# Performance work log

Hardware: AMD Instinct MI355X
Metric: run time of the kernel (lower is better)

## Reference

```python
import jax, jax.numpy as jnp
import numpy as np

B, S, N = 1, 256, 384
MSA_S, Z_D = 64, 128
H, C_H = 8, 32
C_OPM = 32
INF = 1e9

def ln(x, w, b):
    mu = jnp.mean(x, -1, keepdims=True)
    var = jnp.mean(jnp.square(x - mu), -1, keepdims=True)
    return (x - mu) * jax.lax.rsqrt(var + 1e-5) * w + b

def setup_inputs() -> dict:
    key = jax.random.key(0)
    ks = jax.random.split(key, 16)
    def lin(k, out_d, in_d):
        return jax.random.normal(k, (out_d, in_d), jnp.float32) / np.sqrt(in_d)
    return {
        "z": jax.random.normal(ks[0], (B, N, N, Z_D), jnp.float32),
        "m": jax.random.normal(ks[1], (B, S, N, MSA_S), jnp.float32),
        "token_mask": jnp.ones((B, N, N), jnp.float32),
        "msa_mask": jnp.ones((B, S, N), jnp.float32),
        "norm_z_w": jnp.ones((Z_D,), jnp.float32), "norm_z_b": jnp.zeros((Z_D,), jnp.float32),
        "proj_z_w": lin(ks[2], H, Z_D),
        "norm_m_w": jnp.ones((MSA_S,), jnp.float32), "norm_m_b": jnp.zeros((MSA_S,), jnp.float32),
        "proj_m_w": lin(ks[3], H * C_H, MSA_S),
        "proj_g_w": lin(ks[4], H * C_H, MSA_S),
        "pwa_proj_o_w": lin(ks[5], MSA_S, H * C_H),
        "trans_norm_w": jnp.ones((MSA_S,), jnp.float32), "trans_norm_b": jnp.zeros((MSA_S,), jnp.float32),
        "fc1_w": lin(ks[6], 4 * MSA_S, MSA_S),
        "fc2_w": lin(ks[7], 4 * MSA_S, MSA_S),
        "fc3_w": lin(ks[8], MSA_S, 4 * MSA_S),
        "opm_norm_w": jnp.ones((MSA_S,), jnp.float32), "opm_norm_b": jnp.zeros((MSA_S,), jnp.float32),
        "proj_a_w": lin(ks[9], C_OPM, MSA_S),
        "proj_b_w": lin(ks[10], C_OPM, MSA_S),
        "opm_proj_o_w": lin(ks[11], Z_D, C_OPM * C_OPM),
        "opm_proj_o_b": jnp.zeros((Z_D,), jnp.float32),
    }

def reference(z, m, token_mask, msa_mask,
              norm_z_w, norm_z_b, proj_z_w,
              norm_m_w, norm_m_b, proj_m_w, proj_g_w, pwa_proj_o_w,
              trans_norm_w, trans_norm_b, fc1_w, fc2_w, fc3_w,
              opm_norm_w, opm_norm_b, proj_a_w, proj_b_w, opm_proj_o_w, opm_proj_o_b):
    # --- PairWeightedAveraging: pair-biased, gated MSA row attention ---
    b_full = ln(z, norm_z_w, norm_z_b) @ proj_z_w.T                     # [B,N,N,H]
    bias = jnp.transpose(b_full, (0, 3, 1, 2)) + (1.0 - token_mask[:, None]) * (-INF)
    w = jax.nn.softmax(bias, axis=-1)                                   # [B,H,N,N]
    mn = ln(m, norm_m_w, norm_m_b)
    v = (mn @ proj_m_w.T).reshape(B, S, N, H, C_H)                      # [B,S,N,H,c]
    g = jax.nn.sigmoid(mn @ proj_g_w.T)                                 # [B,S,N,H*c]
    o = jnp.einsum('bhij,bsjhd->bsihd', w, v).reshape(B, S, N, H * C_H)
    m = m + (g * o) @ pwa_proj_o_w.T
    # --- MSA transition (SwiGLU) ---
    tn = ln(m, trans_norm_w, trans_norm_b)
    m = m + (jax.nn.silu(tn @ fc1_w.T) * (tn @ fc2_w.T)) @ fc3_w.T
    # --- OuterProductMean -> pair update ---
    mk = msa_mask[..., None]                                            # [B,S,N,1]
    on = ln(m, opm_norm_w, opm_norm_b)
    a = (on @ proj_a_w.T) * mk                                          # [B,S,N,c]
    bb = (on @ proj_b_w.T) * mk                                         # [B,S,N,c]
    num_mask = jnp.clip(jnp.einsum('bsi,bsj->bij', msa_mask, msa_mask), 1.0, None)[..., None]
    opm = jnp.einsum('bsic,bsjd->bijcd', a, bb).reshape(B, N, N, C_OPM * C_OPM) / num_mask
    z = z + opm @ opm_proj_o_w.T + opm_proj_o_b
    return (z, m)
```

## Files before the change

kernel.cpp:

```cpp
#include <hip/hip_runtime.h>
#include <math.h>

constexpr int NRES = 384;
constexpr int NSEQ = 256;
constexpr int DM   = 64;
constexpr int DZ   = 128;
constexpr int NH   = 8;
constexpr int DH   = 32;
constexpr int HC   = NH * DH;
constexpr int DOP  = 32;
constexpr int FF   = 4 * DM;

constexpr int NPAIR = NRES * NRES;
constexpr int NROWS = NSEQ * NRES;
constexpr int ZTOT  = NPAIR * DZ;
constexpr int SD    = NSEQ * DH;
constexpr int ICHUNK = 96;

typedef unsigned short ushort_t;
typedef __attribute__((ext_vector_type(8))) short short8;
typedef __attribute__((ext_vector_type(4))) float f32x4;

__device__ __forceinline__ float wred_sum(float v) {
    #pragma unroll
    for (int off = 32; off; off >>= 1) v += __shfl_xor(v, off, 64);
    return v;
}
__device__ __forceinline__ float sigm(float x) { return 1.0f / (1.0f + expf(-x)); }
__device__ __forceinline__ ushort_t cvt_bf(float f) {
    unsigned u = __float_as_uint(f);
    unsigned r = (u + 0x7FFFu + ((u >> 16) & 1u)) >> 16;
    return (ushort_t)r;
}
__device__ __forceinline__ float cvt_f(ushort_t h) {
    return __uint_as_float(((unsigned)h) << 16);
}
__device__ __forceinline__ f32x4 mfma16(short8 a, short8 b, f32x4 c) {
    return __builtin_amdgcn_mfma_f32_16x16x32_bf16(a, b, c, 0, 0, 0);
}
__device__ __forceinline__ void gld16(const ushort_t* g, ushort_t* l) {
    __builtin_amdgcn_global_load_lds(
        (const __attribute__((address_space(1))) unsigned int*)g,
        (__attribute__((address_space(3))) unsigned int*)l, 16, 0, 0);
}

__global__ __launch_bounds__(256) void k_prep(const float* __restrict__ f1,
                                              const float* __restrict__ f2,
                                              const float* __restrict__ f3,
                                              const float* __restrict__ opW,
                                              const float* __restrict__ pmw,
                                              const float* __restrict__ pgw,
                                              const float* __restrict__ pow_,
                                              const float* __restrict__ paw,
                                              const float* __restrict__ pbw,
                                              const float* __restrict__ pzw,
                                              ushort_t* __restrict__ f1b,
                                              ushort_t* __restrict__ f2b,
                                              ushort_t* __restrict__ f3b,
                                              ushort_t* __restrict__ opWb,
                                              ushort_t* __restrict__ pmwb,
                                              ushort_t* __restrict__ pgwb,
                                              ushort_t* __restrict__ powb,
                                              ushort_t* __restrict__ abwb,
                                              ushort_t* __restrict__ pzwb) {
    int i = blockIdx.x * 256 + threadIdx.x;
    opWb[i] = cvt_bf(opW[i]);
    if (i < FF * DM) {
        f1b[i] = cvt_bf(f1[i]);
        f2b[i] = cvt_bf(f2[i]);
        f3b[i] = cvt_bf(f3[i]);
    }
    if (i < HC * DM) {
        pmwb[i] = cvt_bf(pmw[i]);
        pgwb[i] = cvt_bf(pgw[i]);
        powb[i] = cvt_bf(pow_[i]);
    }
    if (i < 2 * DOP * DM) {
        abwb[i] = cvt_bf(i < DOP * DM ? paw[i] : pbw[i - DOP * DM]);
    }
    if (i < 16 * DZ) {
        pzwb[i] = (i < NH * DZ) ? cvt_bf(pzw[i]) : (ushort_t)0;
    }
}

__global__ __launch_bounds__(256) void k_biassm(const float* __restrict__ z,
                                                const float* __restrict__ nzw,
                                                const float* __restrict__ nzb,
                                                const ushort_t* __restrict__ pzwb,
                                                const float* __restrict__ tmask,
                                                ushort_t* __restrict__ wsb) {
    int i = blockIdx.x;
    __shared__ ushort_t Azl[128][136];
    __shared__ ushort_t Bl[16][136];
    __shared__ float ob[8][388];
    __shared__ float wln[128], bln[128];
    int t = threadIdx.x;
    if (t < 128) { wln[t] = nzw[t]; bln[t] = nzb[t]; }
    int wave = t >> 6, lane = t & 63;
    int lk = (lane >> 4) * 8, lr = lane & 15;
    int wr = wave * 32;
    for (int idx = t * 8; idx < 16 * DZ; idx += 256 * 8) {
        int row = idx >> 7, col = idx & 127;
        *(short8*)&Bl[row][col] = *(const short8*)&pzwb[idx];
    }
    __syncthreads();
    for (int c = 0; c < 3; c++) {
        {
            int jl = t >> 1, cb = (t & 1) * 64;
            const float* src = &z[((size_t)i * NRES + c * 128 + jl) * DZ + cb];
            float4 v[16];
            float s1 = 0.0f, s2 = 0.0f;
            #pragma unroll
            for (int q = 0; q < 16; q++) {
                v[q] = *(const float4*)&src[q * 4];
                s1 += v[q].x + v[q].y + v[q].z + v[q].w;
                s2 += v[q].x * v[q].x + v[q].y * v[q].y + v[q].z * v[q].z + v[q].w * v[q].w;
            }
            s1 += __shfl_xor(s1, 1, 64);
            s2 += __shfl_xor(s2, 1, 64);
            float mu = s1 * (1.0f / 128.0f);
            float var = s2 * (1.0f / 128.0f) - mu * mu;
            float rs = rsqrtf(var + 1e-5f);
            #pragma unroll
            for (int q = 0; q < 8; q++) {
                float4 xa = v[2 * q], xb = v[2 * q + 1];
                int base = cb + q * 8;
                short8 o;
                o[0] = (short)cvt_bf((xa.x - mu) * rs * wln[base + 0] + bln[base + 0]);
                o[1] = (short)cvt_bf((xa.y - mu) * rs * wln[base + 1] + bln[base + 1]);
                o[2] = (short)cvt_bf((xa.z - mu) * rs * wln[base + 2] + bln[base + 2]);
                o[3] = (short)cvt_bf((xa.w - mu) * rs * wln[base + 3] + bln[base + 3]);
                o[4] = (short)cvt_bf((xb.x - mu) * rs * wln[base + 4] + bln[base + 4]);
                o[5] = (short)cvt_bf((xb.y - mu) * rs * wln[base + 5] + bln[base + 5]);
                o[6] = (short)cvt_bf((xb.z - mu) * rs * wln[base + 6] + bln[base + 6]);
                o[7] = (short)cvt_bf((xb.w - mu) * rs * wln[base + 7] + bln[base + 7]);
                *(short8*)&Azl[jl][base] = o;
            }
        }
        __syncthreads();
        f32x4 acc[2] = {};
        #pragma unroll
        for (int ks = 0; ks < 4; ks++) {
            short8 b = *(const short8*)&Bl[lr][ks * 32 + lk];
            short8 a0 = *(const short8*)&Azl[wr + lr][ks * 32 + lk];
            short8 a1 = *(const short8*)&Azl[wr + 16 + lr][ks * 32 + lk];
            acc[0] = mfma16(a0, b, acc[0]);
            acc[1] = mfma16(a1, b, acc[1]);
        }
        if (lr < NH) {
            #pragma unroll
            for (int ri = 0; ri < 2; ri++) {
                int jb = c * 128 + wr + 16 * ri + (lane >> 4) * 4;
                #pragma unroll
                for (int r = 0; r < 4; r++)
                    ob[lr][jb + r] = acc[ri][r];
            }
        }
        __syncthreads();
    }
    int h = wave * 2 + (lane >> 5);
    int l32 = lane & 31;
    int jb = l32 * 12;
    const float* tm = &tmask[(size_t)i * NRES];
    float vals[12];
    float mx = -1e30f;
    #pragma unroll
    for (int q = 0; q < 12; q++) {
        float v = ob[h][jb + q] + (1.0f - tm[jb + q]) * (-1e9f);
        vals[q] = v;
        mx = fmaxf(mx, v);
    }
    #pragma unroll
    for (int off = 16; off; off >>= 1) mx = fmaxf(mx, __shfl_xor(mx, off, 64));
    float sum = 0.0f;
    #pragma unroll
    for (int q = 0; q < 12; q++) { vals[q] = expf(vals[q] - mx); sum += vals[q]; }
    #pragma unroll
    for (int off = 16; off; off >>= 1) sum += __shfl_xor(sum, off, 64);
    float inv = 1.0f / sum;
    ushort_t* o = &wsb[(size_t)h * NPAIR + (size_t)i * NRES + jb];
    #pragma unroll
    for (int q = 0; q < 12; q++) o[q] = cvt_bf(vals[q] * inv);
}

__global__ __launch_bounds__(256) void k_ln64(const float* __restrict__ src,
                                              const float* __restrict__ lw,
                                              const float* __restrict__ lb,
                                              ushort_t* __restrict__ dst) {
    int wave = threadIdx.x >> 6, lane = threadIdx.x & 63;
    int r = blockIdx.x * 4 + wave;
    float x = src[(size_t)r * DM + lane];
    float mu = wred_sum(x) * (1.0f / 64.0f);
    float d = x - mu;
    float var = wred_sum(d * d) * (1.0f / 64.0f);
    dst[(size_t)r * DM + lane] = cvt_bf(d * rsqrtf(var + 1e-5f) * lw[lane] + lb[lane]);
}

__global__ __launch_bounds__(256) void k_vproj_mfma(const ushort_t* __restrict__ A,
                                                    const ushort_t* __restrict__ Bt,
                                                    ushort_t* __restrict__ vtt) {
    int m0 = blockIdx.y * 64, n0c = blockIdx.x * 64;
    __shared__ ushort_t Al[64][40];
    __shared__ ushort_t Bl[64][40];
    __shared__ ushort_t ot[64][72];
    int t = threadIdx.x;
    int srow = t >> 2, sko = (t & 3) * 8;
    int wave = t >> 6, lane = t & 63;
    int wr = (wave >> 1) * 32, wc = (wave & 1) * 32;
    int lk = (lane >> 4) * 8, lr = lane & 15;
    f32x4 acc[2][2] = {};
    for (int k0 = 0; k0 < DM; k0 += 32) {
        *(short8*)&Al[srow][sko] = *(const short8*)&A[(size_t)(m0 + srow) * DM + k0 + sko];
        *(short8*)&Bl[srow][sko] = *(const short8*)&Bt[(size_t)(n0c + srow) * DM + k0 + sko];
        __syncthreads();
        short8 a0 = *(const short8*)&Al[wr + lr][lk];
        short8 a1 = *(const short8*)&Al[wr + 16 + lr][lk];
        short8 b0 = *(const short8*)&Bl[wc + lr][lk];
        short8 b1 = *(const short8*)&Bl[wc + 16 + lr][lk];
        acc[0][0] = mfma16(a0, b0, acc[0][0]);
        acc[0][1] = mfma16(a0, b1, acc[0][1]);
        acc[1][0] = mfma16(a1, b0, acc[1][0]);
        acc[1][1] = mfma16(a1, b1, acc[1][1]);
        __syncthreads();
    }
    #pragma unroll
    for (int ri = 0; ri < 2; ri++)
        #pragma unroll
        for (int ci = 0; ci < 2; ci++) {
            int rowb = wr + 16 * ri + (lane >> 4) * 4;
            int colb = wc + 16 * ci + lr;
            #pragma unroll
            for (int r = 0; r < 4; r++)
                ot[colb][rowb + r] = cvt_bf(acc[ri][ci][r]);
        }
    __syncthreads();
    int s = m0 / NRES, n0 = m0 % NRES;
    int h0 = n0c >> 5;
    int orow = t >> 2, seg = (t & 3) * 16;
    short8 v0 = *(const short8*)&ot[orow][seg];
    short8 v1 = *(const short8*)&ot[orow][seg + 8];
    int hh = orow >> 5, dd = orow & 31;
    ushort_t* dst = &vtt[(((size_t)(h0 + hh) * SD) + s * DH + dd) * NRES + n0 + seg];
    *(short8*)&dst[0] = v0;
    *(short8*)&dst[8] = v1;
}

__global__ __launch_bounds__(256) void k_tr(const ushort_t* __restrict__ src,
                                            ushort_t* __restrict__ dst,
                                            int R, int C) {
    size_t bs = (size_t)R * C;
    const ushort_t* s = src + blockIdx.z * bs;
    ushort_t* d = dst + blockIdx.z * bs;
    int r0 = blockIdx.y * 64, c0 = blockIdx.x * 64;
    __shared__ ushort_t tile[64][72];
    int t = threadIdx.x;
    int tr = t >> 2, tc = (t & 3) * 16;
    *(short8*)&tile[tr][tc]     = *(const short8*)&s[(size_t)(r0 + tr) * C + c0 + tc];
    *(short8*)&tile[tr][tc + 8] = *(const short8*)&s[(size_t)(r0 + tr) * C + c0 + tc + 8];
    __syncthreads();
    short8 o0, o1;
    #pragma unroll
    for (int i = 0; i < 8; i++) {
        o0[i] = (short)tile[tc + i][tr];
        o1[i] = (short)tile[tc + 8 + i][tr];
    }
    *(short8*)&d[(size_t)(c0 + tr) * R + r0 + tc]     = o0;
    *(short8*)&d[(size_t)(c0 + tr) * R + r0 + tc + 8] = o1;
}

__global__ __launch_bounds__(256) void k_attn_mfma(const ushort_t* __restrict__ wsb,
                                                   const ushort_t* __restrict__ vtt,
                                                   ushort_t* __restrict__ otb2) {
    int h = blockIdx.z;
    const ushort_t* A  = wsb + (size_t)h * NPAIR;
    const ushort_t* Bt = vtt + (size_t)h * SD * NRES;
    int m0 = blockIdx.y * 128, n0 = blockIdx.x * 128;
    __shared__ ushort_t Al[128 * 32];
    __shared__ ushort_t Bl[128 * 32];
    int t = threadIdx.x;
    int w = t >> 6, lane = t & 63;
    int wr = (w >> 1) * 64, wc = (w & 1) * 64;
    int lq = lane >> 4, lr = lane & 15;
    int rS = w * 16 + (lane >> 2);
    int cqs = (((lane & 3) ^ ((rS >> 1) & 3)) << 3);
    f32x4 acc[4][4] = {};
    for (int k0 = 0; k0 < NRES; k0 += 32) {
        gld16(&A [(size_t)(m0 + rS)      * NRES + k0 + cqs], &Al[(w * 16) * 32]);
        gld16(&A [(size_t)(m0 + 64 + rS) * NRES + k0 + cqs], &Al[(64 + w * 16) * 32]);
        gld16(&Bt[(size_t)(n0 + rS)      * NRES + k0 + cqs], &Bl[(w * 16) * 32]);
        gld16(&Bt[(size_t)(n0 + 64 + rS) * NRES + k0 + cqs], &Bl[(64 + w * 16) * 32]);
        __syncthreads();
        short8 af[4], bf2[4];
        #pragma unroll
        for (int i = 0; i < 4; i++) {
            int ra = wr + 16 * i + lr;
            int rb = wc + 16 * i + lr;
            af[i]  = *(const short8*)&Al[ra * 32 + ((lq ^ ((ra >> 1) & 3)) << 3)];
            bf2[i] = *(const short8*)&Bl[rb * 32 + ((lq ^ ((rb >> 1) & 3)) << 3)];
        }
        #pragma unroll
        for (int ri = 0; ri < 4; ri++)
            #pragma unroll
            for (int ci = 0; ci < 4; ci++)
                acc[ri][ci] = mfma16(af[ri], bf2[ci], acc[ri][ci]);
        __syncthreads();
    }
    #pragma unroll
    for (int ri = 0; ri < 4; ri++)
        #pragma unroll
        for (int ci = 0; ci < 4; ci++) {
            int row0 = m0 + wr + 16 * ri + (lane >> 4) * 4;
            int col  = n0 + wc + 16 * ci + lr;
            int s = col >> 5, dd = col & 31;
            #pragma unroll
            for (int r = 0; r < 4; r++)
                otb2[((size_t)s * NRES + row0 + r) * HC + h * DH + dd] = cvt_bf(acc[ri][ci][r]);
        }
}

__global__ __launch_bounds__(256) void k_gateout(const ushort_t* __restrict__ A,
                                                 const ushort_t* __restrict__ Bg,
                                                 const ushort_t* __restrict__ otb2,
                                                 const ushort_t* __restrict__ Bo,
                                                 const float* __restrict__ m,
                                                 float* __restrict__ mout) {
    int m0 = blockIdx.x * 64;
    __shared__ ushort_t Al[64][72];
    __shared__ ushort_t Bl[64][72];
    __shared__ ushort_t go[64][264];
    int t = threadIdx.x;
    int srow = t >> 2, sko = (t & 3) * 16;
    int wave = t >> 6, lane = t & 63;
    int wr = (wave >> 1) * 32, wc = (wave & 1) * 32;
    int lk = (lane >> 4) * 8, lr = lane & 15;
    {
        const ushort_t* arow = &A[(size_t)(m0 + srow) * DM + sko];
        *(short8*)&Al[srow][sko]     = *(const short8*)&arow[0];
        *(short8*)&Al[srow][sko + 8] = *(const short8*)&arow[8];
    }
    __syncthreads();
    short8 a[2][2];
    a[0][0] = *(const short8*)&Al[wr + lr][lk];
    a[0][1] = *(const short8*)&Al[wr + lr][32 + lk];
    a[1][0] = *(const short8*)&Al[wr + 16 + lr][lk];
    a[1][1] = *(const short8*)&Al[wr + 16 + lr][32 + lk];
    for (int nq = 0; nq < 4; nq++) {
        __syncthreads();
        {
            const ushort_t* brow = &Bg[(size_t)(nq * 64 + srow) * DM + sko];
            *(short8*)&Bl[srow][sko]     = *(const short8*)&brow[0];
            *(short8*)&Bl[srow][sko + 8] = *(const short8*)&brow[8];
        }
        __syncthreads();
        f32x4 acc[2][2] = {};
        #pragma unroll
        for (int ks = 0; ks < 2; ks++) {
            short8 b0 = *(const short8*)&Bl[wc + lr][ks * 32 + lk];
            short8 b1 = *(const short8*)&Bl[wc + 16 + lr][ks * 32 + lk];
            acc[0][0] = mfma16(a[0][ks], b0, acc[0][0]);
            acc[0][1] = mfma16(a[0][ks], b1, acc[0][1]);
            acc[1][0] = mfma16(a[1][ks], b0, acc[1][0]);
            acc[1][1] = mfma16(a[1][ks], b1, acc[1][1]);
        }
        #pragma unroll
        for (int ri = 0; ri < 2; ri++)
            #pragma unroll
            for (int ci = 0; ci < 2; ci++) {
                int lrow = wr + 16 * ri + (lane >> 4) * 4;
                int col  = nq * 64 + wc + 16 * ci + lr;
                #pragma unroll
                for (int r = 0; r < 4; r++) {
                    float ov = cvt_f(otb2[(size_t)(m0 + lrow + r) * HC + col]);
                    go[lrow + r][col] = cvt_bf(sigm(acc[ri][ci][r]) * ov);
                }
            }
    }
    f32x4 acc[2][2] = {};
    for (int k0 = 0; k0 < HC; k0 += 32) {
        __syncthreads();
        *(short8*)&Bl[t >> 2][(t & 3) * 8] = *(const short8*)&Bo[(size_t)(t >> 2) * HC + k0 + (t & 3) * 8];
        __syncthreads();
        short8 a0 = *(const short8*)&go[wr + lr][k0 + lk];
        short8 a1 = *(const short8*)&go[wr + 16 + lr][k0 + lk];
        short8 b0 = *(const short8*)&Bl[wc + lr][lk];
        short8 b1 = *(const short8*)&Bl[wc + 16 + lr][lk];
        acc[0][0] = mfma16(a0, b0, acc[0][0]);
        acc[0][1] = mfma16(a0, b1, acc[0][1]);
        acc[1][0] = mfma16(a1, b0, acc[1][0]);
        acc[1][1] = mfma16(a1, b1, acc[1][1]);
    }
    #pragma unroll
    for (int ri = 0; ri < 2; ri++)
        #pragma unroll
        for (int ci = 0; ci < 2; ci++) {
            int row0 = m0 + wr + 16 * ri + (lane >> 4) * 4;
            int col  = wc + 16 * ci + lr;
            #pragma unroll
            for (int r = 0; r < 4; r++) {
                size_t idx = (size_t)(row0 + r) * DM + col;
                mout[idx] = m[idx] + acc[ri][ci][r];
            }
        }
}

__global__ __launch_bounds__(256) void k_fctrans(const ushort_t* __restrict__ A,
                                                 const ushort_t* __restrict__ B1,
                                                 const ushort_t* __restrict__ B2,
                                                 const ushort_t* __restrict__ B3,
                                                 float* __restrict__ mio) {
    int m0 = blockIdx.x * 64;
    __shared__ ushort_t Al[64][72];
    __shared__ ushort_t B1l[64][72];
    __shared__ ushort_t B2l[64][72];
    __shared__ ushort_t hhl[64][264];
    int t = threadIdx.x;
    int srow = t >> 2, sko = (t & 3) * 16;
    int wave = t >> 6, lane = t & 63;
    int wr = (wave >> 1) * 32, wc = (wave & 1) * 32;
    int lk = (lane >> 4) * 8, lr = lane & 15;
    {
        const ushort_t* arow = &A[(size_t)(m0 + srow) * DM + sko];
        *(short8*)&Al[srow][sko]     = *(const short8*)&arow[0];
        *(short8*)&Al[srow][sko + 8] = *(const short8*)&arow[8];
    }
    __syncthreads();
    short8 a[2][2];
    a[0][0] = *(const short8*)&Al[wr + lr][lk];
    a[0][1] = *(const short8*)&Al[wr + lr][32 + lk];
    a[1][0] = *(const short8*)&Al[wr + 16 + lr][lk];
    a[1][1] = *(const short8*)&Al[wr + 16 + lr][32 + lk];
    for (int nq = 0; nq < 4; nq++) {
        __syncthreads();
        {
            const ushort_t* b1r = &B1[(size_t)(nq * 64 + srow) * DM + sko];
            const ushort_t* b2r = &B2[(size_t)(nq * 64 + srow) * DM + sko];
            *(short8*)&B1l[srow][sko]     = *(const short8*)&b1r[0];
            *(short8*)&B1l[srow][sko + 8] = *(const short8*)&b1r[8];
            *(short8*)&B2l[srow][sko]     = *(const short8*)&b2r[0];
            *(short8*)&B2l[srow][sko + 8] = *(const short8*)&b2r[8];
        }
        __syncthreads();
        f32x4 acc1[2][2] = {}, acc2[2][2] = {};
        #pragma unroll
        for (int ks = 0; ks < 2; ks++) {
            short8 p0 = *(const short8*)&B1l[wc + lr][ks * 32 + lk];
            short8 p1 = *(const short8*)&B1l[wc + 16 + lr][ks * 32 + lk];
            short8 q0 = *(const short8*)&B2l[wc + lr][ks * 32 + lk];
            short8 q1 = *(const short8*)&B2l[wc + 16 + lr][ks * 32 + lk];
            acc1[0][0] = mfma16(a[0][ks], p0, acc1[0][0]);
            acc1[0][1] = mfma16(a[0][ks], p1, acc1[0][1]);
            acc1[1][0] = mfma16(a[1][ks], p0, acc1[1][0]);
            acc1[1][1] = mfma16(a[1][ks], p1, acc1[1][1]);
            acc2[0][0] = mfma16(a[0][ks], q0, acc2[0][0]);
            acc2[0][1] = mfma16(a[0][ks], q1, acc2[0][1]);
            acc2[1][0] = mfma16(a[1][ks], q0, acc2[1][0]);
            acc2[1][1] = mfma16(a[1][ks], q1, acc2[1][1]);
        }
        #pragma unroll
        for (int ri = 0; ri < 2; ri++)
            #pragma unroll
            for (int ci = 0; ci < 2; ci++) {
                int lrow = wr + 16 * ri + (lane >> 4) * 4;
                int col  = nq * 64 + wc + 16 * ci + lr;
                #pragma unroll
                for (int r = 0; r < 4; r++) {
                    float a1v = acc1[ri][ci][r], a2v = acc2[ri][ci][r];
                    hhl[lrow + r][col] = cvt_bf(a1v * sigm(a1v) * a2v);
                }
            }
    }
    f32x4 acc[2][2] = {};
    for (int k0 = 0; k0 < FF; k0 += 32) {
        __syncthreads();
        *(short8*)&B1l[t >> 2][(t & 3) * 8] = *(const short8*)&B3[(size_t)(t >> 2) * FF + k0 + (t & 3) * 8];
        __syncthreads();
        short8 a0 = *(const short8*)&hhl[wr + lr][k0 + lk];
        short8 a1 = *(const short8*)&hhl[wr + 16 + lr][k0 + lk];
        short8 b0 = *(const short8*)&B1l[wc + lr][lk];
        short8 b1 = *(const short8*)&B1l[wc + 16 + lr][lk];
        acc[0][0] = mfma16(a0, b0, acc[0][0]);
        acc[0][1] = mfma16(a0, b1, acc[0][1]);
        acc[1][0] = mfma16(a1, b0, acc[1][0]);
        acc[1][1] = mfma16(a1, b1, acc[1][1]);
    }
    #pragma unroll
    for (int ri = 0; ri < 2; ri++)
        #pragma unroll
        for (int ci = 0; ci < 2; ci++) {
            int row0 = m0 + wr + 16 * ri + (lane >> 4) * 4;
            int col  = wc + 16 * ci + lr;
            #pragma unroll
            for (int r = 0; r < 4; r++)
                mio[(size_t)(row0 + r) * DM + col] += acc[ri][ci][r];
        }
}

__global__ __launch_bounds__(256) void k_ab_mfma(const ushort_t* __restrict__ A,
                                                 const ushort_t* __restrict__ Bt,
                                                 const float* __restrict__ smask,
                                                 ushort_t* __restrict__ abuf,
                                                 ushort_t* __restrict__ bbuf) {
    int m0 = blockIdx.x * 64;
    __shared__ ushort_t Al[64][40];
    __shared__ ushort_t Bl[64][40];
    int t = threadIdx.x;
    int srow = t >> 2, sko = (t & 3) * 8;
    int wave = t >> 6, lane = t & 63;
    int wr = (wave >> 1) * 32, wc = (wave & 1) * 32;
    int lk = (lane >> 4) * 8, lr = lane & 15;
    f32x4 acc[2][2] = {};
    for (int k0 = 0; k0 < DM; k0 += 32) {
        *(short8*)&Al[srow][sko] = *(const short8*)&A[(size_t)(m0 + srow) * DM + k0 + sko];
        *(short8*)&Bl[srow][sko] = *(const short8*)&Bt[(size_t)srow * DM + k0 + sko];
        __syncthreads();
        short8 a0 = *(const short8*)&Al[wr + lr][lk];
        short8 a1 = *(const short8*)&Al[wr + 16 + lr][lk];
        short8 b0 = *(const short8*)&Bl[wc + lr][lk];
        short8 b1 = *(const short8*)&Bl[wc + 16 + lr][lk];
        acc[0][0] = mfma16(a0, b0, acc[0][0]);
        acc[0][1] = mfma16(a0, b1, acc[0][1]);
        acc[1][0] = mfma16(a1, b0, acc[1][0]);
        acc[1][1] = mfma16(a1, b1, acc[1][1]);
        __syncthreads();
    }
    #pragma unroll
    for (int ri = 0; ri < 2; ri++)
        #pragma unroll
        for (int ci = 0; ci < 2; ci++) {
            int row0 = m0 + wr + 16 * ri + (lane >> 4) * 4;
            int col  = wc + 16 * ci + lr;
            #pragma unroll
            for (int r = 0; r < 4; r++) {
                int rr = row0 + r;
                int s = rr / NRES, n = rr % NRES;
                float v = acc[ri][ci][r] * smask[rr];
                if (col < DOP)
                    abuf[(size_t)s * (NRES * DOP) + n * DOP + col] = cvt_bf(v);
                else
                    bbuf[(size_t)s * (NRES * DOP) + n * DOP + (col - DOP)] = cvt_bf(v);
            }
        }
}

__global__ __launch_bounds__(256) void k_msum(const float* __restrict__ smask,
                                              float* __restrict__ msum) {
    int i0 = blockIdx.y * 64, j0 = blockIdx.x * 64;
    __shared__ float As[16][64];
    __shared__ float Bs[16][64];
    int t = threadIdx.x;
    int ty = t >> 4, tx = t & 15;
    float acc[4][4] = {};
    for (int k0 = 0; k0 < NSEQ; k0 += 16) {
        int kk = t >> 4, x4 = (t & 15) * 4;
        *(float4*)&As[kk][x4] = *(const float4*)&smask[(size_t)(k0 + kk) * NRES + i0 + x4];
        *(float4*)&Bs[kk][x4] = *(const float4*)&smask[(size_t)(k0 + kk) * NRES + j0 + x4];
        __syncthreads();
        #pragma unroll
        for (int k = 0; k < 16; k++) {
            float4 a4 = *(const float4*)&As[k][ty * 4];
            float4 b4 = *(const float4*)&Bs[k][tx * 4];
            float ar[4] = {a4.x, a4.y, a4.z, a4.w};
            float br[4] = {b4.x, b4.y, b4.z, b4.w};
            #pragma unroll
            for (int i2 = 0; i2 < 4; i2++)
                #pragma unroll
                for (int j2 = 0; j2 < 4; j2++)
                    acc[i2][j2] += ar[i2] * br[j2];
        }
        __syncthreads();
    }
    #pragma unroll
    for (int r = 0; r < 4; r++) {
        float4 o4 = make_float4(fmaxf(acc[r][0], 1.0f), fmaxf(acc[r][1], 1.0f),
                                fmaxf(acc[r][2], 1.0f), fmaxf(acc[r][3], 1.0f));
        *(float4*)&msum[(size_t)(i0 + ty * 4 + r) * NRES + j0 + tx * 4] = o4;
    }
}

__global__ __launch_bounds__(256) void k_opm_mfma(const ushort_t* __restrict__ At,
                                                  const ushort_t* __restrict__ Bt,
                                                  ushort_t* __restrict__ opmc) {
    int m0 = blockIdx.y * 128;
    int n0 = blockIdx.x * 128;
    __shared__ ushort_t Al[128 * 32];
    __shared__ ushort_t Bl[128 * 32];
    int t = threadIdx.x;
    int w = t >> 6, lane = t & 63;
    int wr = (w >> 1) * 64, wc = (w & 1) * 64;
    int lq = lane >> 4, lr = lane & 15;
    int rS = w * 16 + (lane >> 2);
    int cqs = (((lane & 3) ^ ((rS >> 1) & 3)) << 3);
    f32x4 acc[4][4] = {};
    for (int k0 = 0; k0 < NSEQ; k0 += 32) {
        gld16(&At[(size_t)(m0 + rS)      * NSEQ + k0 + cqs], &Al[(w * 16) * 32]);
        gld16(&At[(size_t)(m0 + 64 + rS) * NSEQ + k0 + cqs], &Al[(64 + w * 16) * 32]);
        gld16(&Bt[(size_t)(n0 + rS)      * NSEQ + k0 + cqs], &Bl[(w * 16) * 32]);
        gld16(&Bt[(size_t)(n0 + 64 + rS) * NSEQ + k0 + cqs], &Bl[(64 + w * 16) * 32]);
        __syncthreads();
        short8 af[4], bf2[4];
        #pragma unroll
        for (int i = 0; i < 4; i++) {
            int ra = wr + 16 * i + lr;
            int rb = wc + 16 * i + lr;
            af[i]  = *(const short8*)&Al[ra * 32 + ((lq ^ ((ra >> 1) & 3)) << 3)];
            bf2[i] = *(const short8*)&Bl[rb * 32 + ((lq ^ ((rb >> 1) & 3)) << 3)];
        }
        #pragma unroll
        for (int ri = 0; ri < 4; ri++)
            #pragma unroll
            for (int ci = 0; ci < 4; ci++)
                acc[ri][ci] = mfma16(af[ri], bf2[ci], acc[ri][ci]);
        __syncthreads();
    }
    #pragma unroll
    for (int ri = 0; ri < 4; ri++)
        #pragma unroll
        for (int ci = 0; ci < 4; ci++) {
            int mb = m0 + wr + 16 * ri + (lane >> 4) * 4;
            int n  = n0 + wc + 16 * ci + lr;
            int j = n >> 5, dd = n & 31;
            #pragma unroll
            for (int r = 0; r < 4; r++) {
                int mm = mb + r;
                int il = mm >> 5, c = mm & 31;
                opmc[((size_t)(il * NRES + j) << 10) + (c << 5) + dd] = cvt_bf(acc[ri][ci][r]);
            }
        }
}

__global__ __launch_bounds__(256) void k_proj_mfma(const ushort_t* __restrict__ A,
                                                   const ushort_t* __restrict__ Bt,
                                                   const float* __restrict__ opB,
                                                   const float* __restrict__ msum,
                                                   const float* __restrict__ zin,
                                                   float* __restrict__ zout,
                                                   int ib) {
    int m0 = blockIdx.x * 128;
    __shared__ ushort_t Al[128 * 32];
    __shared__ ushort_t Bl[128 * 32];
    int t = threadIdx.x;
    int w = t >> 6, lane = t & 63;
    int wr = (w >> 1) * 64, wc = (w & 1) * 64;
    int lq = lane >> 4, lr = lane & 15;
    int rS = w * 16 + (lane >> 2);
    int cqs = (((lane & 3) ^ ((rS >> 1) & 3)) << 3);
    f32x4 acc[4][4] = {};
    for (int k0 = 0; k0 < 1024; k0 += 32) {
        gld16(&A [(size_t)(m0 + rS)      * 1024 + k0 + cqs], &Al[(w * 16) * 32]);
        gld16(&A [(size_t)(m0 + 64 + rS) * 1024 + k0 + cqs], &Al[(64 + w * 16) * 32]);
        gld16(&Bt[(size_t)(rS)           * 1024 + k0 + cqs], &Bl[(w * 16) * 32]);
        gld16(&Bt[(size_t)(64 + rS)      * 1024 + k0 + cqs], &Bl[(64 + w * 16) * 32]);
        __syncthreads();
        short8 af[4], bf2[4];
        #pragma unroll
        for (int i = 0; i < 4; i++) {
            int ra = wr + 16 * i + lr;
            int rb = wc + 16 * i + lr;
            af[i]  = *(const short8*)&Al[ra * 32 + ((lq ^ ((ra >> 1) & 3)) << 3)];
            bf2[i] = *(const short8*)&Bl[rb * 32 + ((lq ^ ((rb >> 1) & 3)) << 3)];
        }
        #pragma unroll
        for (int ri = 0; ri < 4; ri++)
            #pragma unroll
            for (int ci = 0; ci < 4; ci++)
                acc[ri][ci] = mfma16(af[ri], bf2[ci], acc[ri][ci]);
        __syncthreads();
    }
    #pragma unroll
    for (int ri = 0; ri < 4; ri++)
        #pragma unroll
        for (int ci = 0; ci < 4; ci++) {
            int row0 = m0 + wr + 16 * ri + (lane >> 4) * 4;
            int col  = wc + 16 * ci + lr;
            #pragma unroll
            for (int r = 0; r < 4; r++) {
                size_t G = (size_t)ib * NRES + row0 + r;
                float inv = 1.0f / msum[G];
                zout[G * DZ + col] = zin[G * DZ + col] + acc[ri][ci][r] * inv + opB[col];
            }
        }
}

extern "C" void kernel_launch(void* const* d_in, const int* in_sizes, int n_in,
                              void* d_out, int out_size, void* d_ws, size_t ws_size,
                              hipStream_t stream) {
    const float* z     = (const float*)d_in[0];
    const float* m     = (const float*)d_in[1];
    const float* tmask = (const float*)d_in[2];
    const float* smask = (const float*)d_in[3];
    const float* nzw   = (const float*)d_in[4];
    const float* nzb   = (const float*)d_in[5];
    const float* pzw   = (const float*)d_in[6];
    const float* nmw   = (const float*)d_in[7];
    const float* nmb   = (const float*)d_in[8];
    const float* pmw   = (const float*)d_in[9];
    const float* pgw   = (const float*)d_in[10];
    const float* pow_  = (const float*)d_in[11];
    const float* tnw   = (const float*)d_in[12];
    const float* tnb_  = (const float*)d_in[13];
    const float* f1    = (const float*)d_in[14];
    const float* f2    = (const float*)d_in[15];
    const float* f3    = (const float*)d_in[16];
    const float* onw   = (const float*)d_in[17];
    const float* onb   = (const float*)d_in[18];
    const float* paw   = (const float*)d_in[19];
    const float* pbw   = (const float*)d_in[20];
    const float* opW   = (const float*)d_in[21];
    const float* opB   = (const float*)d_in[22];

    float* zout = (float*)d_out;
    float* mout = zout + ZTOT;

    char* W = (char*)d_ws;
    ushort_t* wsb  = (ushort_t*)(W + 4718592);
    ushort_t* mnb  = (ushort_t*)(W + 7077888);
    ushort_t* vtR  = (ushort_t*)(W + 19660800);
    ushort_t* vtt  = (ushort_t*)(W + 69992448);
    ushort_t* otb2 = (ushort_t*)(W + 120324096);
    float*    msum = (float*)(W + 170655744);
    ushort_t* f1b  = (ushort_t*)(W + 171245568);
    ushort_t* f2b  = (ushort_t*)(W + 171278336);
    ushort_t* f3b  = (ushort_t*)(W + 171311104);
    ushort_t* opWb = (ushort_t*)(W + 171343872);
    ushort_t* pmwb = (ushort_t*)(W + 171606016);
    ushort_t* pgwb = (ushort_t*)(W + 171638784);
    ushort_t* powb = (ushort_t*)(W + 171671552);
    ushort_t* abwb = (ushort_t*)(W + 171704320);
    ushort_t* pzwb = (ushort_t*)(W + 171712512);
    ushort_t* tn_bf = vtt;
    ushort_t* onb_bf = mnb;
    ushort_t* abuf = (ushort_t*)(W + 69992448 + 12582912);
    ushort_t* bbuf = (ushort_t*)(W + 69992448 + 18874368);
    ushort_t* abt  = otb2;
    ushort_t* bbt  = (ushort_t*)(W + 120324096 + 6291456);
    ushort_t* opmc = vtR;

    k_prep<<<512, 256, 0, stream>>>(f1, f2, f3, opW, pmw, pgw, pow_, paw, pbw, pzw,
                                    f1b, f2b, f3b, opWb, pmwb, pgwb, powb, abwb, pzwb);

    k_biassm<<<NRES, 256, 0, stream>>>(z, nzw, nzb, pzwb, tmask, wsb);
    k_ln64<<<NROWS / 4, 256, 0, stream>>>(m, nmw, nmb, mnb);
    k_vproj_mfma<<<dim3(HC / 64, NROWS / 64), 256, 0, stream>>>(mnb, pmwb, vtt);
    k_attn_mfma<<<dim3(SD / 128, NRES / 128, NH), 256, 0, stream>>>(wsb, vtt, otb2);
    k_gateout<<<NROWS / 64, 256, 0, stream>>>(mnb, pgwb, otb2, powb, m, mout);

    k_ln64<<<NROWS / 4, 256, 0, stream>>>(mout, tnw, tnb_, tn_bf);
    k_fctrans<<<NROWS / 64, 256, 0, stream>>>(tn_bf, f1b, f2b, f3b, mout);

    k_ln64<<<NROWS / 4, 256, 0, stream>>>(mout, onw, onb, onb_bf);
    k_ab_mfma<<<NROWS / 64, 256, 0, stream>>>(onb_bf, abwb, smask, abuf, bbuf);
    k_tr<<<dim3((NRES * DOP) / 64, NSEQ / 64, 2), 256, 0, stream>>>(abuf, abt, NSEQ, NRES * DOP);
    k_msum<<<dim3(NRES / 64, NRES / 64), 256, 0, stream>>>(smask, msum);
    for (int cb = 0; cb < NRES / ICHUNK; cb++) {
        int ib = cb * ICHUNK;
        const ushort_t* Achunk = abt + (size_t)(ib * DOP) * NSEQ;
        k_opm_mfma<<<dim3((NRES * DOP) / 128, (ICHUNK * DOP) / 128), 256, 0, stream>>>(Achunk, bbt, opmc);
        k_proj_mfma<<<(ICHUNK * NRES) / 128, 256, 0, stream>>>(opmc, opWb, opB, msum, z, zout, ib);
    }
}
```

Baseline: 499.9 us.

## Fuse outer-product GEMM with output projection, keeping opm tile in LDS

Merges the chunked OPM outer-product GEMM and the 1024->128 projection into one kernel. Each 128x128 outer-product tile (16 residue pairs x 1024 features) is staged in swizzled shared memory and projected straight to z, so the bf16 opm intermediate never goes to global memory and the per-chunk launches disappear. The attention kernel also swaps MFMA operand order so each lane holds contiguous output columns and can store packed 4-element vectors. The risk is that the fused projection reads the opW weights directly from global memory in every block, and the extra shared memory may lower occupancy.

```diff
diff --git a/kernel.cpp b/kernel.cpp
--- a/kernel.cpp
+++ b/kernel.cpp
@@ -15,10 +15,10 @@
 constexpr int NROWS = NSEQ * NRES;
 constexpr int ZTOT  = NPAIR * DZ;
 constexpr int SD    = NSEQ * DH;
-constexpr int ICHUNK = 96;
 
 typedef unsigned short ushort_t;
 typedef __attribute__((ext_vector_type(8))) short short8;
+typedef __attribute__((ext_vector_type(4))) short short4_t;
 typedef __attribute__((ext_vector_type(4))) float f32x4;
 
 __device__ __forceinline__ float wred_sum(float v) {
@@ -302,19 +302,20 @@
         for (int ri = 0; ri < 4; ri++)
             #pragma unroll
             for (int ci = 0; ci < 4; ci++)
-                acc[ri][ci] = mfma16(af[ri], bf2[ci], acc[ri][ci]);
+                acc[ri][ci] = mfma16(bf2[ci], af[ri], acc[ri][ci]);
         __syncthreads();
     }
     #pragma unroll
     for (int ri = 0; ri < 4; ri++)
         #pragma unroll
         for (int ci = 0; ci < 4; ci++) {
-            int row0 = m0 + wr + 16 * ri + (lane >> 4) * 4;
-            int col  = n0 + wc + 16 * ci + lr;
-            int s = col >> 5, dd = col & 31;
-            #pragma unroll
-            for (int r = 0; r < 4; r++)
-                otb2[((size_t)s * NRES + row0 + r) * HC + h * DH + dd] = cvt_bf(acc[ri][ci][r]);
+            int i_row = m0 + wr + 16 * ri + lr;
+            int nl = n0 + wc + 16 * ci + lq * 4;
+            int s = nl >> 5, dd = nl & 31;
+            short4_t pk;
+            #pragma unroll
+            for (int r = 0; r < 4; r++) pk[r] = (short)cvt_bf(acc[ri][ci][r]);
+            *(short4_t*)&otb2[((size_t)s * NRES + i_row) * HC + h * DH + dd] = pk;
         }
 }
 
@@ -577,13 +578,18 @@
     }
 }
 
-__global__ __launch_bounds__(256) void k_opm_mfma(const ushort_t* __restrict__ At,
-                                                  const ushort_t* __restrict__ Bt,
-                                                  ushort_t* __restrict__ opmc) {
+__global__ __launch_bounds__(256) void k_opmproj(const ushort_t* __restrict__ At,
+                                                 const ushort_t* __restrict__ Bt,
+                                                 const ushort_t* __restrict__ Wb,
+                                                 const float* __restrict__ opB,
+                                                 const float* __restrict__ msum,
+                                                 const float* __restrict__ zin,
+                                                 float* __restrict__ zout) {
     int m0 = blockIdx.y * 128;
     int n0 = blockIdx.x * 128;
     __shared__ ushort_t Al[128 * 32];
     __shared__ ushort_t Bl[128 * 32];
+    __shared__ ushort_t opml[16][1048];
     int t = threadIdx.x;
     int w = t >> 6, lane = t & 63;
     int wr = (w >> 1) * 64, wc = (w & 1) * 64;
@@ -609,76 +615,56 @@
         for (int ri = 0; ri < 4; ri++)
             #pragma unroll
             for (int ci = 0; ci < 4; ci++)
-                acc[ri][ci] = mfma16(af[ri], bf2[ci], acc[ri][ci]);
+                acc[ri][ci] = mfma16(bf2[ci], af[ri], acc[ri][ci]);
         __syncthreads();
     }
     #pragma unroll
     for (int ri = 0; ri < 4; ri++)
         #pragma unroll
         for (int ci = 0; ci < 4; ci++) {
-            int mb = m0 + wr + 16 * ri + (lane >> 4) * 4;
-            int n  = n0 + wc + 16 * ci + lr;
-            int j = n >> 5, dd = n & 31;
-            #pragma unroll
-            for (int r = 0; r < 4; r++) {
-                int mm = mb + r;
-                int il = mm >> 5, c = mm & 31;
-                opmc[((size_t)(il * NRES + j) << 10) + (c << 5) + dd] = cvt_bf(acc[ri][ci][r]);
-            }
-        }
-}
-
-__global__ __launch_bounds__(256) void k_proj_mfma(const ushort_t* __restrict__ A,
-                                                   const ushort_t* __restrict__ Bt,
-                                                   const float* __restrict__ opB,
-                                                   const float* __restrict__ msum,
-                                                   const float* __restrict__ zin,
-                                                   float* __restrict__ zout,
-                                                   int ib) {
-    int m0 = blockIdx.x * 128;
-    __shared__ ushort_t Al[128 * 32];
-    __shared__ ushort_t Bl[128 * 32];
-    int t = threadIdx.x;
-    int w = t >> 6, lane = t & 63;
-    int wr = (w >> 1) * 64, wc = (w & 1) * 64;
-    int lq = lane >> 4, lr = lane & 15;
-    int rS = w * 16 + (lane >> 2);
-    int cqs = (((lane & 3) ^ ((rS >> 1) & 3)) << 3);
-    f32x4 acc[4][4] = {};
+            int mll = wr + 16 * ri + lr;
+            int il = mll >> 5, c = mll & 31;
+            int nll = wc + 16 * ci + lq * 4;
+            int j = nll >> 5, d = nll & 31;
+            int p = il * 4 + j;
+            int k = c * 32 + d;
+            int kk = k ^ ((c & 3) << 3);
+            short4_t pk;
+            #pragma unroll
+            for (int r = 0; r < 4; r++) pk[r] = (short)cvt_bf(acc[ri][ci][r]);
+            *(short4_t*)&opml[p][kk] = pk;
+        }
+    __syncthreads();
+    f32x4 facc[2] = {};
+    #pragma unroll 4
     for (int k0 = 0; k0 < 1024; k0 += 32) {
-        gld16(&A [(size_t)(m0 + rS)      * 1024 + k0 + cqs], &Al[(w * 16) * 32]);
-        gld16(&A [(size_t)(m0 + 64 + rS) * 1024 + k0 + cqs], &Al[(64 + w * 16) * 32]);
-        gld16(&Bt[(size_t)(rS)           * 1024 + k0 + cqs], &Bl[(w * 16) * 32]);
-        gld16(&Bt[(size_t)(64 + rS)      * 1024 + k0 + cqs], &Bl[(64 + w * 16) * 32]);
-        __syncthreads();
-        short8 af[4], bf2[4];
-        #pragma unroll
-        for (int i = 0; i < 4; i++) {
-            int ra = wr + 16 * i + lr;
-            int rb = wc + 16 * i + lr;
-            af[i]  = *(const short8*)&Al[ra * 32 + ((lq ^ ((ra >> 1) & 3)) << 3)];
-            bf2[i] = *(const short8*)&Bl[rb * 32 + ((lq ^ ((rb >> 1) & 3)) << 3)];
-        }
-        #pragma unroll
-        for (int ri = 0; ri < 4; ri++)
-            #pragma unroll
-            for (int ci = 0; ci < 4; ci++)
-                acc[ri][ci] = mfma16(af[ri], bf2[ci], acc[ri][ci]);
-        __syncthreads();
-    }
-    #pragma unroll
-    for (int ri = 0; ri < 4; ri++)
-        #pragma unroll
-        for (int ci = 0; ci < 4; ci++) {
-            int row0 = m0 + wr + 16 * ri + (lane >> 4) * 4;
-            int col  = wc + 16 * ci + lr;
-            #pragma unroll
-            for (int r = 0; r < 4; r++) {
-                size_t G = (size_t)ib * NRES + row0 + r;
-                float inv = 1.0f / msum[G];
-                zout[G * DZ + col] = zin[G * DZ + col] + acc[ri][ci][r] * inv + opB[col];
-            }
-        }
+        int kidx = k0 + lq * 8;
+        int cc = kidx >> 5;
+        short8 ap = *(const short8*)&opml[lr][kidx ^ ((cc & 3) << 3)];
+        #pragma unroll
+        for (int ci = 0; ci < 2; ci++) {
+            int e = w * 32 + 16 * ci + lr;
+            short8 be = *(const short8*)&Wb[(size_t)e * 1024 + kidx];
+            facc[ci] = mfma16(be, ap, facc[ci]);
+        }
+    }
+    int p = lr;
+    int iG = (m0 >> 5) + (p >> 2);
+    int jG = (n0 >> 5) + (p & 3);
+    size_t G = (size_t)iG * NRES + jG;
+    float inv = 1.0f / msum[G];
+    #pragma unroll
+    for (int ci = 0; ci < 2; ci++) {
+        int e0 = w * 32 + 16 * ci + lq * 4;
+        float4 zv = *(const float4*)&zin[G * DZ + e0];
+        float4 bv = *(const float4*)&opB[e0];
+        float4 o4;
+        o4.x = zv.x + facc[ci][0] * inv + bv.x;
+        o4.y = zv.y + facc[ci][1] * inv + bv.y;
+        o4.z = zv.z + facc[ci][2] * inv + bv.z;
+        o4.w = zv.w + facc[ci][3] * inv + bv.w;
+        *(float4*)&zout[G * DZ + e0] = o4;
+    }
 }
 
 extern "C" void kernel_launch(void* const* d_in, const int* in_sizes, int n_in,
@@ -714,9 +700,14 @@
     char* W = (char*)d_ws;
     ushort_t* wsb  = (ushort_t*)(W + 4718592);
     ushort_t* mnb  = (ushort_t*)(W + 7077888);
-    ushort_t* vtR  = (ushort_t*)(W + 19660800);
     ushort_t* vtt  = (ushort_t*)(W + 69992448);
     ushort_t* otb2 = (ushort_t*)(W + 120324096);
+    ushort_t* tn_bf  = vtt;
+    ushort_t* onb_bf = mnb;
+    ushort_t* abuf = (ushort_t*)(W + 69992448 + 12582912);
+    ushort_t* bbuf = (ushort_t*)(W + 69992448 + 18874368);
+    ushort_t* abt  = otb2;
+    ushort_t* bbt  = (ushort_t*)(W + 120324096 + 6291456);
     float*    msum = (float*)(W + 170655744);
     ushort_t* f1b  = (ushort_t*)(W + 171245568);
     ushort_t* f2b  = (ushort_t*)(W + 171278336);
@@ -727,13 +718,6 @@
     ushort_t* powb = (ushort_t*)(W + 171671552);
     ushort_t* abwb = (ushort_t*)(W + 171704320);
     ushort_t* pzwb = (ushort_t*)(W + 171712512);
-    ushort_t* tn_bf = vtt;
-    ushort_t* onb_bf = mnb;
-    ushort_t* abuf = (ushort_t*)(W + 69992448 + 12582912);
-    ushort_t* bbuf = (ushort_t*)(W + 69992448 + 18874368);
-    ushort_t* abt  = otb2;
-    ushort_t* bbt  = (ushort_t*)(W + 120324096 + 6291456);
-    ushort_t* opmc = vtR;
 
     k_prep<<<512, 256, 0, stream>>>(f1, f2, f3, opW, pmw, pgw, pow_, paw, pbw, pzw,
                                     f1b, f2b, f3b, opWb, pmwb, pgwb, powb, abwb, pzwb);
@@ -751,10 +735,5 @@
     k_ab_mfma<<<NROWS / 64, 256, 0, stream>>>(onb_bf, abwb, smask, abuf, bbuf);
     k_tr<<<dim3((NRES * DOP) / 64, NSEQ / 64, 2), 256, 0, stream>>>(abuf, abt, NSEQ, NRES * DOP);
     k_msum<<<dim3(NRES / 64, NRES / 64), 256, 0, stream>>>(smask, msum);
-    for (int cb = 0; cb < NRES / ICHUNK; cb++) {
-        int ib = cb * ICHUNK;
-        const ushort_t* Achunk = abt + (size_t)(ib * DOP) * NSEQ;
-        k_opm_mfma<<<dim3((NRES * DOP) / 128, (ICHUNK * DOP) / 128), 256, 0, stream>>>(Achunk, bbt, opmc);
-        k_proj_mfma<<<(ICHUNK * NRES) / 128, 256, 0, stream>>>(opmc, opWb, opB, msum, z, zout, ib);
-    }
-}
+    k_opmproj<<<dim3(96, 96), 256, 0, stream>>>(abt, bbt, opWb, opB, msum, z, zout);
+}
```

New measurement: 582.6 us. +16.5%, slower.
